# Optimization experiments

Hardware: AMD Instinct MI355X
Metric: run time of the kernel (lower is better)

Reference implementation:

```python
import jax, jax.numpy as jnp
import numpy as np

N, E, NG = 50000, 800000, 256          # nodes, edges, graphs
NODE, EDGE, HID, OUT = 64, 16, 64, 1   # feature dims
NUM_LAYERS = 3


def _lin(key, fan_in, fan_out):
    # torch Linear default init: U(-1/sqrt(fan_in), 1/sqrt(fan_in))
    kw, kb = jax.random.split(key)
    bound = 1.0 / np.sqrt(fan_in)
    W = jax.random.uniform(kw, (fan_in, fan_out), jnp.float32, -bound, bound)
    b = jax.random.uniform(kb, (fan_out,), jnp.float32, -bound, bound)
    return W, b


def setup_inputs() -> dict:
    key = jax.random.key(0)
    ks = jax.random.split(key, 8)
    x = jax.random.normal(ks[0], (N, NODE), jnp.float32)
    edge_attr = jax.random.normal(ks[1], (E, EDGE), jnp.float32)
    edge_index = jax.random.randint(ks[2], (2, E), 0, N, dtype=jnp.int32)
    batch = jnp.sort(jax.random.randint(ks[3], (N,), 0, NG, dtype=jnp.int32))
    W_nh, b_nh = _lin(ks[4], NODE, HID)                 # node_to_hidden
    W_mh, b_mh = _lin(ks[5], 2 * HID + EDGE, HID)       # message_to_hidden
    W_om, b_om = _lin(ks[6], 2 * HID + NODE, HID)       # outMsgLin
    W_out, b_out = _lin(ks[7], HID, OUT)                # outLin
    return {"x": x, "edge_attr": edge_attr,
            "W_nh": W_nh, "b_nh": b_nh, "W_mh": W_mh, "b_mh": b_mh,
            "W_om": W_om, "b_om": b_om, "W_out": W_out, "b_out": b_out,
            "edge_index": edge_index, "batch": batch}


def reference(x, edge_attr, W_nh, b_nh, W_mh, b_mh, W_om, b_om, W_out, b_out,
              edge_index, batch):
    # h0 = relu(node_to_hidden(x))
    h0 = jax.nn.relu(x @ W_nh + b_nh)                      # [N, HID]

    # add_self_loops: append N self edges, self-loop edge_attr filled with 1.0
    self_idx = jnp.arange(N, dtype=edge_index.dtype)
    src = jnp.concatenate([edge_index[0], self_idx])       # x_j index (source)
    dst = jnp.concatenate([edge_index[1], self_idx])       # x_i index (target)
    ea = jnp.concatenate([edge_attr,
                          jnp.ones((N, EDGE), edge_attr.dtype)], axis=0)

    # MPN: num_layers of gather-concat -> scatter-add -> linear + h0 -> relu
    h = h0
    for _ in range(NUM_LAYERS):
        msg = jnp.concatenate([h[dst], h[src], ea], axis=1)        # [E+N, 2H+EDGE]
        agg = jax.ops.segment_sum(msg, dst, num_segments=N)        # [N, 2H+EDGE]
        h = jax.nn.relu(agg @ W_mh + b_mh + h0)                    # [N, HID]

    # outMsg: message = concat[h_i, h_j, x_j], aggr add, update identity
    out_msg = jnp.concatenate([h[dst], h[src], x[src]], axis=1)    # [E+N, 2H+NODE]
    agg2 = jax.ops.segment_sum(out_msg, dst, num_segments=N)       # [N, 2H+NODE]

    out = jax.nn.relu(agg2 @ W_om + b_om)                          # [N, HID]
    pooled = jax.ops.segment_sum(out, batch, num_segments=NG)      # [NG, HID]
    return pooled @ W_out + b_out                                  # [NG, OUT]
```

## Files before the change

### kernel.cpp

```cpp
#include <hip/hip_runtime.h>
#include <hip/hip_fp16.h>

#define N_NODES 50000
#define N_EDGES 800000
#define NGRAPH  256
#define FDIM    64
#define EDIM    16
#define NT      (N_NODES / 16)
#define SH      8
#define M8      (N_NODES * SH)
#define NB8     ((M8 + 255) / 256)
#define CH8     ((NB8 + 255) / 256)
#define NBG     ((N_NODES + 31) / 32)

using half8  = __attribute__((ext_vector_type(8))) _Float16;
using float4v = __attribute__((ext_vector_type(4))) float;

__device__ __forceinline__ unsigned hadd2u(unsigned a, unsigned b) {
    __half2 r = __hadd2(__builtin_bit_cast(__half2, a), __builtin_bit_cast(__half2, b));
    return __builtin_bit_cast(unsigned, r);
}
__device__ __forceinline__ unsigned hmul2u(unsigned a, __half2 m) {
    __half2 r = __hmul2(__builtin_bit_cast(__half2, a), m);
    return __builtin_bit_cast(unsigned, r);
}


__global__ void k_count(const int* __restrict__ dst, int* __restrict__ cnt8) {
    int e = blockIdx.x * blockDim.x + threadIdx.x;
    if (e < N_EDGES) atomicAdd(&cnt8[dst[e] * SH + (e & (SH - 1))], 1);
}

__global__ void k_cvt_x(const float* __restrict__ x, __half* __restrict__ x16) {
    int t = blockIdx.x * blockDim.x + threadIdx.x;
    if (t < N_NODES * FDIM) x16[t] = __float2half(x[t]);
}

__global__ void k_blksum(const int* __restrict__ cnt8, int* __restrict__ blksum) {
    __shared__ int red[4];
    int b = blockIdx.x, t = threadIdx.x;
    int idx = b * 256 + t;
    int s = (idx < M8) ? cnt8[idx] : 0;
#pragma unroll
    for (int off = 32; off > 0; off >>= 1) s += __shfl_down(s, off, 64);
    int lane = t & 63, wid = t >> 6;
    if (lane == 0) red[wid] = s;
    __syncthreads();
    if (t == 0) blksum[b] = red[0] + red[1] + red[2] + red[3];
}

__global__ void k_scanblk(const int* __restrict__ blksum, int* __restrict__ boff,
                          int* __restrict__ rowp8) {
    __shared__ int sh[256];
    int t = threadIdx.x;
    int base = t * CH8;
    int v[CH8];
    int s = 0;
#pragma unroll
    for (int i = 0; i < CH8; i++) {
        int idx = base + i;
        v[i] = (idx < NB8) ? blksum[idx] : 0;
        s += v[i];
    }
    sh[t] = s;
    __syncthreads();
    for (int off = 1; off < 256; off <<= 1) {
        int u = (t >= off) ? sh[t - off] : 0;
        __syncthreads();
        sh[t] += u;
        __syncthreads();
    }
    int run = (t == 0) ? 0 : sh[t - 1];
#pragma unroll
    for (int i = 0; i < CH8; i++) {
        int idx = base + i;
        if (idx < NB8) boff[idx] = run;
        run += v[i];
    }
    if (t == 255) rowp8[M8] = sh[255];
}

__global__ void k_rowp(const int* __restrict__ cnt8, const int* __restrict__ boff,
                       int* __restrict__ rowp8, int* __restrict__ cur8) {
    __shared__ int sh[256];
    int b = blockIdx.x, t = threadIdx.x;
    int idx = b * 256 + t;
    int v = (idx < M8) ? cnt8[idx] : 0;
    sh[t] = v;
    __syncthreads();
    for (int off = 1; off < 256; off <<= 1) {
        int u = (t >= off) ? sh[t - off] : 0;
        __syncthreads();
        sh[t] += u;
        __syncthreads();
    }
    if (idx < M8) {
        int excl = sh[t] - v + boff[b];
        rowp8[idx] = excl;
        cur8[idx]  = excl;
    }
}

__global__ void k_degf(const int* __restrict__ rowp8, float* __restrict__ degf) {
    int i = blockIdx.x * blockDim.x + threadIdx.x;
    if (i < N_NODES) degf[i] = (float)(rowp8[(i + 1) * SH] - rowp8[i * SH] + 1);
}

__global__ void k_fill(const int* __restrict__ src, const int* __restrict__ dst,
                       int* __restrict__ cur8, int2* __restrict__ colperm) {
    int e = blockIdx.x * blockDim.x + threadIdx.x;
    if (e < N_EDGES) {
        int pos = atomicAdd(&cur8[dst[e] * SH + (e & (SH - 1))], 1);
        colperm[pos] = make_int2(src[e], e);
    }
}


__global__ __launch_bounds__(256, 8) void k_gather(
    const __half* __restrict__ h16,
    const int* __restrict__ rowp8, const int2* __restrict__ colperm,
    __half* __restrict__ agg16) {
    int lane = threadIdx.x & 63, wid = threadIdx.x >> 6;
    int g = lane >> 3;
    int c = lane & 7;
    const uint4* h8 = (const uint4*)h16;
    int node = (blockIdx.x * 4 + wid) * 8 + g;
    if (node >= N_NODES) return;
    int beg = rowp8[node * SH], end = rowp8[(node + 1) * SH];
    float a0 = 0, a1 = 0, a2 = 0, a3 = 0, a4 = 0, a5 = 0, a6 = 0, a7 = 0;
    for (int p = beg; p < end; p += 8) {
        int cidx = p + c; if (cidx > end - 1) cidx = end - 1;
        int vj = colperm[cidx].x;
#pragma unroll
        for (int k = 0; k < 8; k++) {
            int j = __shfl(vj, g * 8 + k, 64);
            if (p + k < end) {
                uint4 v = h8[(size_t)j * 8 + c];
                float2 f0 = __half22float2(__builtin_bit_cast(__half2, v.x));
                float2 f1 = __half22float2(__builtin_bit_cast(__half2, v.y));
                float2 f2 = __half22float2(__builtin_bit_cast(__half2, v.z));
                float2 f3 = __half22float2(__builtin_bit_cast(__half2, v.w));
                a0 += f0.x; a1 += f0.y; a2 += f1.x; a3 += f1.y;
                a4 += f2.x; a5 += f2.y; a6 += f3.x; a7 += f3.y;
            }
        }
    }
    uint4 o;
    o.x = __builtin_bit_cast(unsigned, __floats2half2_rn(a0, a1));
    o.y = __builtin_bit_cast(unsigned, __floats2half2_rn(a2, a3));
    o.z = __builtin_bit_cast(unsigned, __floats2half2_rn(a4, a5));
    o.w = __builtin_bit_cast(unsigned, __floats2half2_rn(a6, a7));
    ((uint4*)agg16)[(size_t)node * 8 + c] = o;
}

__global__ __launch_bounds__(256, 8) void k_ea_agg(
    const float* __restrict__ edge_attr,
    const int* __restrict__ rowp8, const int2* __restrict__ colperm,
    float* __restrict__ ea) {
    int lane = threadIdx.x & 63, wid = threadIdx.x >> 6;
    int g = lane >> 3;
    int c = lane & 7;
    const float2* a2p = (const float2*)edge_attr;
    int node = (blockIdx.x * 4 + wid) * 8 + g;
    if (node >= N_NODES) return;
    int beg = rowp8[node * SH], end = rowp8[(node + 1) * SH];
    float x0 = 0.f, x1 = 0.f;
    for (int p = beg; p < end; p += 8) {
        int cidx = p + c; if (cidx > end - 1) cidx = end - 1;
        int vj = colperm[cidx].y;
#pragma unroll
        for (int k = 0; k < 8; k++) {
            int e = __shfl(vj, g * 8 + k, 64);
            if (p + k < end) {
                float2 v = a2p[(size_t)e * 8 + c];
                x0 += v.x; x1 += v.y;
            }
        }
    }
    ((float2*)ea)[(size_t)node * 8 + c] = make_float2(x0, x1);
}

__global__ void k_h0base(const float* __restrict__ x, const float* __restrict__ ea,
                         const float* __restrict__ Wnh, const float* __restrict__ bnh,
                         const float* __restrict__ Wmh, const float* __restrict__ bmh,
                         __half* __restrict__ h0out16, __half* __restrict__ base16) {
    __shared__ __align__(16) float sx[4][FDIM];
    __shared__ __align__(16) float sea[4][EDIM];
    int lane = threadIdx.x & 63;
    int wid  = threadIdx.x >> 6;
    float wnh[FDIM], w3[EDIM];
#pragma unroll
    for (int m = 0; m < FDIM; m++) wnh[m] = Wnh[m * FDIM + lane];
    float csum = 0.f;
#pragma unroll
    for (int m = 0; m < EDIM; m++) {
        w3[m] = Wmh[(2 * FDIM + m) * FDIM + lane];
        csum += w3[m];
    }
    float bnhk = bnh[lane], bmhk = bmh[lane];
    int gw = blockIdx.x * 4 + wid;
    int nw = gridDim.x * 4;
    for (int i = gw; i < N_NODES; i += nw) {
        sx[wid][lane] = x[i * FDIM + lane];
        if (lane < EDIM) sea[wid][lane] = ea[i * EDIM + lane];
        float acc0 = bnhk, acc1 = 0.f, acc2 = 0.f, acc3 = 0.f;
        const float4* s4 = (const float4*)sx[wid];
#pragma unroll
        for (int m4 = 0; m4 < FDIM / 4; m4++) {
            float4 v = s4[m4];
            acc0 = fmaf(v.x, wnh[4 * m4 + 0], acc0);
            acc1 = fmaf(v.y, wnh[4 * m4 + 1], acc1);
            acc2 = fmaf(v.z, wnh[4 * m4 + 2], acc2);
            acc3 = fmaf(v.w, wnh[4 * m4 + 3], acc3);
        }
        float h0 = fmaxf((acc0 + acc2) + (acc1 + acc3), 0.f);
        float b0 = h0 + bmhk + csum, b1 = 0.f, b2 = 0.f, b3 = 0.f;
        const float4* e4 = (const float4*)sea[wid];
#pragma unroll
        for (int m4 = 0; m4 < EDIM / 4; m4++) {
            float4 v = e4[m4];
            b0 = fmaf(v.x, w3[4 * m4 + 0], b0);
            b1 = fmaf(v.y, w3[4 * m4 + 1], b1);
            b2 = fmaf(v.z, w3[4 * m4 + 2], b2);
            b3 = fmaf(v.w, w3[4 * m4 + 3], b3);
        }
        h0out16[i * FDIM + lane] = __float2half(h0);
        base16[i * FDIM + lane]  = __float2half((b0 + b2) + (b1 + b3));
    }
}

#define SROW 136

__global__ __launch_bounds__(256, 4) void k_mv_mfma(
    const __half* __restrict__ agg16, const __half* __restrict__ hin16,
    const __half* __restrict__ base16, const float* __restrict__ degf,
    const float* __restrict__ Wmh, __half* __restrict__ hout16) {
    __shared__ __align__(16) _Float16 S[4][16 * SROW];
    int lane = threadIdx.x & 63, wid = threadIdx.x >> 6;
    int n = lane & 15, quad = lane >> 4;
    half8 bfr[4][4];
#pragma unroll
    for (int kk = 0; kk < 4; kk++)
#pragma unroll
        for (int nn = 0; nn < 4; nn++) {
            half8 tmp;
#pragma unroll
            for (int j = 0; j < 8; j++) {
                int kp = kk * 32 + quad * 8 + j;
                int krow = (kp < 64) ? (64 + kp) : (kp - 64);
                tmp[j] = (_Float16)Wmh[krow * FDIM + nn * 16 + n];
            }
            bfr[kk][nn] = tmp;
        }
    int t = blockIdx.x * 4 + wid;
    if (t >= NT) return;
    int tb = t * 16;
    {
        int m = lane >> 2, c = lane & 3;
        int node = tb + m;
        const uint4* ag4 = (const uint4*)agg16;
        const uint4* hh4 = (const uint4*)hin16;
        uint4 agA = ag4[(size_t)node * 8 + c * 2];
        uint4 agB = ag4[(size_t)node * 8 + c * 2 + 1];
        uint4 hA  = hh4[(size_t)node * 8 + c * 2];
        uint4 hB  = hh4[(size_t)node * 8 + c * 2 + 1];
        __half dh = __float2half(degf[node]);
        __half2 dh2 = __halves2half2(dh, dh);
        uint4 s2A, s2B, s1A, s1B;
        s2A.x = hadd2u(agA.x, hA.x); s2A.y = hadd2u(agA.y, hA.y);
        s2A.z = hadd2u(agA.z, hA.z); s2A.w = hadd2u(agA.w, hA.w);
        s2B.x = hadd2u(agB.x, hB.x); s2B.y = hadd2u(agB.y, hB.y);
        s2B.z = hadd2u(agB.z, hB.z); s2B.w = hadd2u(agB.w, hB.w);
        s1A.x = hmul2u(hA.x, dh2); s1A.y = hmul2u(hA.y, dh2);
        s1A.z = hmul2u(hA.z, dh2); s1A.w = hmul2u(hA.w, dh2);
        s1B.x = hmul2u(hB.x, dh2); s1B.y = hmul2u(hB.y, dh2);
        s1B.z = hmul2u(hB.z, dh2); s1B.w = hmul2u(hB.w, dh2);
        uint4* Sw = (uint4*)(&S[wid][m * SROW]);
        Sw[c * 2]     = s2A;
        Sw[c * 2 + 1] = s2B;
        Sw[8 + c * 2]     = s1A;
        Sw[8 + c * 2 + 1] = s1B;
    }
    float4v acc[4];
#pragma unroll
    for (int nn = 0; nn < 4; nn++)
#pragma unroll
        for (int r = 0; r < 4; r++)
            acc[nn][r] = __half2float(base16[(size_t)(tb + quad * 4 + r) * FDIM + nn * 16 + n]);
    const _Float16* Sr = S[wid];
#pragma unroll
    for (int kk = 0; kk < 4; kk++) {
        half8 a = *(const half8*)(Sr + (lane & 15) * SROW + kk * 32 + quad * 8);
#pragma unroll
        for (int nn = 0; nn < 4; nn++)
            acc[nn] = __builtin_amdgcn_mfma_f32_16x16x32_f16(a, bfr[kk][nn], acc[nn], 0, 0, 0);
    }
#pragma unroll
    for (int nn = 0; nn < 4; nn++)
#pragma unroll
        for (int r = 0; r < 4; r++)
            hout16[(size_t)(tb + quad * 4 + r) * FDIM + nn * 16 + n] =
                __float2half(fmaxf(acc[nn][r], 0.f));
}

__global__ __launch_bounds__(256, 4) void k_out_mv_mfma(
    const __half* __restrict__ agg16, const __half* __restrict__ hin16,
    const __half* __restrict__ obase16, const float* __restrict__ degf,
    const float* __restrict__ Wom, const float* __restrict__ Wout,
    float* __restrict__ sc) {
    __shared__ __align__(16) _Float16 S[4][16 * SROW];
    int lane = threadIdx.x & 63, wid = threadIdx.x >> 6;
    int n = lane & 15, quad = lane >> 4;
    half8 bfr[4][4];
#pragma unroll
    for (int kk = 0; kk < 4; kk++)
#pragma unroll
        for (int nn = 0; nn < 4; nn++) {
            half8 tmp;
#pragma unroll
            for (int j = 0; j < 8; j++) {
                int kp = kk * 32 + quad * 8 + j;
                int krow = (kp < 64) ? (64 + kp) : (kp - 64);
                tmp[j] = (_Float16)Wom[krow * FDIM + nn * 16 + n];
            }
            bfr[kk][nn] = tmp;
        }
    float wo0 = Wout[n], wo1 = Wout[16 + n], wo2 = Wout[32 + n], wo3 = Wout[48 + n];
    int t = blockIdx.x * 4 + wid;
    if (t >= NT) return;
    int tb = t * 16;
    {
        int m = lane >> 2, c = lane & 3;
        int node = tb + m;
        const uint4* ag4 = (const uint4*)agg16;
        const uint4* hh4 = (const uint4*)hin16;
        uint4 agA = ag4[(size_t)node * 8 + c * 2];
        uint4 agB = ag4[(size_t)node * 8 + c * 2 + 1];
        uint4 hA  = hh4[(size_t)node * 8 + c * 2];
        uint4 hB  = hh4[(size_t)node * 8 + c * 2 + 1];
        __half dh = __float2half(degf[node]);
        __half2 dh2 = __halves2half2(dh, dh);
        uint4 s2A, s2B, s1A, s1B;
        s2A.x = hadd2u(agA.x, hA.x); s2A.y = hadd2u(agA.y, hA.y);
        s2A.z = hadd2u(agA.z, hA.z); s2A.w = hadd2u(agA.w, hA.w);
        s2B.x = hadd2u(agB.x, hB.x); s2B.y = hadd2u(agB.y, hB.y);
        s2B.z = hadd2u(agB.z, hB.z); s2B.w = hadd2u(agB.w, hB.w);
        s1A.x = hmul2u(hA.x, dh2); s1A.y = hmul2u(hA.y, dh2);
        s1A.z = hmul2u(hA.z, dh2); s1A.w = hmul2u(hA.w, dh2);
        s1B.x = hmul2u(hB.x, dh2); s1B.y = hmul2u(hB.y, dh2);
        s1B.z = hmul2u(hB.z, dh2); s1B.w = hmul2u(hB.w, dh2);
        uint4* Sw = (uint4*)(&S[wid][m * SROW]);
        Sw[c * 2]     = s2A;
        Sw[c * 2 + 1] = s2B;
        Sw[8 + c * 2]     = s1A;
        Sw[8 + c * 2 + 1] = s1B;
    }
    float4v acc[4];
#pragma unroll
    for (int nn = 0; nn < 4; nn++)
#pragma unroll
        for (int r = 0; r < 4; r++)
            acc[nn][r] = __half2float(obase16[(size_t)(tb + quad * 4 + r) * FDIM + nn * 16 + n]);
    const _Float16* Sr = S[wid];
#pragma unroll
    for (int kk = 0; kk < 4; kk++) {
        half8 a = *(const half8*)(Sr + (lane & 15) * SROW + kk * 32 + quad * 8);
#pragma unroll
        for (int nn = 0; nn < 4; nn++)
            acc[nn] = __builtin_amdgcn_mfma_f32_16x16x32_f16(a, bfr[kk][nn], acc[nn], 0, 0, 0);
    }
#pragma unroll
    for (int r = 0; r < 4; r++) {
        float s = fmaxf(acc[0][r], 0.f) * wo0 + fmaxf(acc[1][r], 0.f) * wo1
                + fmaxf(acc[2][r], 0.f) * wo2 + fmaxf(acc[3][r], 0.f) * wo3;
        s += __shfl_xor(s, 1, 64);
        s += __shfl_xor(s, 2, 64);
        s += __shfl_xor(s, 4, 64);
        s += __shfl_xor(s, 8, 64);
        if (n == 0) sc[tb + quad * 4 + r] = s;
    }
}

#define SROW2 72
__global__ __launch_bounds__(256, 4) void k_obase_mfma(
    const __half* __restrict__ aggX16, const __half* __restrict__ x16,
    const float* __restrict__ Wom, const float* __restrict__ bom,
    __half* __restrict__ obase16) {
    __shared__ __align__(16) _Float16 S[4][16 * SROW2];
    int lane = threadIdx.x & 63, wid = threadIdx.x >> 6;
    int n = lane & 15, quad = lane >> 4;
    half8 bfr[2][4];
#pragma unroll
    for (int kk = 0; kk < 2; kk++)
#pragma unroll
        for (int nn = 0; nn < 4; nn++) {
            half8 tmp;
#pragma unroll
            for (int j = 0; j < 8; j++) {
                int kp = kk * 32 + quad * 8 + j;
                tmp[j] = (_Float16)Wom[(128 + kp) * FDIM + nn * 16 + n];
            }
            bfr[kk][nn] = tmp;
        }
    float bom_n[4];
#pragma unroll
    for (int nn = 0; nn < 4; nn++) bom_n[nn] = bom[nn * 16 + n];
    int t = blockIdx.x * 4 + wid;
    if (t >= NT) return;
    int tb = t * 16;
    {
        int m = lane >> 2, c = lane & 3;
        int node = tb + m;
        const uint4* ag4 = (const uint4*)aggX16;
        const uint4* xx4 = (const uint4*)x16;
        uint4 agA = ag4[(size_t)node * 8 + c * 2];
        uint4 agB = ag4[(size_t)node * 8 + c * 2 + 1];
        uint4 xA  = xx4[(size_t)node * 8 + c * 2];
        uint4 xB  = xx4[(size_t)node * 8 + c * 2 + 1];
        uint4 sA, sB;
        sA.x = hadd2u(agA.x, xA.x); sA.y = hadd2u(agA.y, xA.y);
        sA.z = hadd2u(agA.z, xA.z); sA.w = hadd2u(agA.w, xA.w);
        sB.x = hadd2u(agB.x, xB.x); sB.y = hadd2u(agB.y, xB.y);
        sB.z = hadd2u(agB.z, xB.z); sB.w = hadd2u(agB.w, xB.w);
        uint4* Sw = (uint4*)(&S[wid][m * SROW2]);
        Sw[c * 2]     = sA;
        Sw[c * 2 + 1] = sB;
    }
    float4v acc[4];
#pragma unroll
    for (int nn = 0; nn < 4; nn++)
#pragma unroll
        for (int r = 0; r < 4; r++) acc[nn][r] = bom_n[nn];
    const _Float16* Sr = S[wid];
#pragma unroll
    for (int kk = 0; kk < 2; kk++) {
        half8 a = *(const half8*)(Sr + (lane & 15) * SROW2 + kk * 32 + quad * 8);
#pragma unroll
        for (int nn = 0; nn < 4; nn++)
            acc[nn] = __builtin_amdgcn_mfma_f32_16x16x32_f16(a, bfr[kk][nn], acc[nn], 0, 0, 0);
    }
#pragma unroll
    for (int nn = 0; nn < 4; nn++)
#pragma unroll
        for (int r = 0; r < 4; r++)
            obase16[(size_t)(tb + quad * 4 + r) * FDIM + nn * 16 + n] =
                __float2half(acc[nn][r]);
}

__global__ void k_pool(const float* __restrict__ sc, const int* __restrict__ batch,
                       const float* __restrict__ b_out, float* __restrict__ out) {
    __shared__ float red[4];
    int g = blockIdx.x, t = threadIdx.x;
    int lo = 0, hi = N_NODES;
    while (lo < hi) { int mid = (lo + hi) >> 1; if (batch[mid] < g) lo = mid + 1; else hi = mid; }
    int lo2 = lo, hi2 = N_NODES;
    while (lo2 < hi2) { int mid = (lo2 + hi2) >> 1; if (batch[mid] < g + 1) lo2 = mid + 1; else hi2 = mid; }
    float s = 0.f;
    for (int i = lo + t; i < lo2; i += 256) s += sc[i];
#pragma unroll
    for (int off = 32; off > 0; off >>= 1) s += __shfl_down(s, off, 64);
    int lane = t & 63, wid = t >> 6;
    if (lane == 0) red[wid] = s;
    __syncthreads();
    if (t == 0) out[g] = red[0] + red[1] + red[2] + red[3] + b_out[0];
}


extern "C" void kernel_launch(void* const* d_in, const int* in_sizes, int n_in,
                              void* d_out, int out_size, void* d_ws, size_t ws_size,
                              hipStream_t stream) {
    const float* x         = (const float*)d_in[0];
    const float* edge_attr = (const float*)d_in[1];
    const float* Wnh       = (const float*)d_in[2];
    const float* bnh       = (const float*)d_in[3];
    const float* Wmh       = (const float*)d_in[4];
    const float* bmh       = (const float*)d_in[5];
    const float* Wom       = (const float*)d_in[6];
    const float* bom       = (const float*)d_in[7];
    const float* Wout      = (const float*)d_in[8];
    const float* bout      = (const float*)d_in[9];
    const int*   eidx      = (const int*)d_in[10];
    const int*   batch     = (const int*)d_in[11];
    const int*   srcI = eidx;
    const int*   dstI = eidx + N_EDGES;
    float* out = (float*)d_out;
    (void)in_sizes; (void)n_in; (void)out_size;

    char* w = (char*)d_ws;
    size_t off = 0;
    auto take = [&](size_t b) -> void* {
        void* p = w + off;
        off = (off + b + 255) & ~(size_t)255;
        return p;
    };
    float*  ea     = (float*)take((size_t)N_NODES * EDIM * 4);
    int*    cnt8   = (int*)take((size_t)M8 * 4);
    int*    rowp8  = (int*)take((size_t)(M8 + 1) * 4);
    int*    cur8   = (int*)take((size_t)M8 * 4);
    float*  degf   = (float*)take((size_t)N_NODES * 4);
    int2*   colperm= (int2*)take((size_t)N_EDGES * 8);
    float*  sc     = (float*)take((size_t)N_NODES * 4);
    int*    blks   = (int*)take((size_t)NB8 * 4);
    int*    boff   = (int*)take((size_t)NB8 * 4);
    __half* x16    = (__half*)take((size_t)N_NODES * FDIM * 2);
    __half* hA16   = (__half*)take((size_t)N_NODES * FDIM * 2);
    __half* hB16   = (__half*)take((size_t)N_NODES * FDIM * 2);
    __half* agg16  = (__half*)take((size_t)N_NODES * FDIM * 2);
    __half* base16 = (__half*)take((size_t)N_NODES * FDIM * 2);
    __half* obase16= (__half*)take((size_t)N_NODES * FDIM * 2);
    (void)ws_size;

    const int MVG = (NT + 3) / 4;
    const int GBG = (NBG + 0);

    hipMemsetAsync(cnt8, 0, (size_t)M8 * 4, stream);
    k_count<<<(N_EDGES + 255) / 256, 256, 0, stream>>>(dstI, cnt8);
    k_cvt_x<<<(N_NODES * FDIM + 255) / 256, 256, 0, stream>>>(x, x16);
    k_blksum<<<NB8, 256, 0, stream>>>(cnt8, blks);
    k_scanblk<<<1, 256, 0, stream>>>(blks, boff, rowp8);
    k_rowp<<<NB8, 256, 0, stream>>>(cnt8, boff, rowp8, cur8);
    k_degf<<<(N_NODES + 255) / 256, 256, 0, stream>>>(rowp8, degf);
    k_fill<<<(N_EDGES + 255) / 256, 256, 0, stream>>>(srcI, dstI, cur8, colperm);

    k_gather<<<GBG, 256, 0, stream>>>(x16, rowp8, colperm, agg16);
    k_obase_mfma<<<MVG, 256, 0, stream>>>(agg16, x16, Wom, bom, obase16);
    k_ea_agg<<<GBG, 256, 0, stream>>>(edge_attr, rowp8, colperm, ea);
    k_h0base<<<2048, 256, 0, stream>>>(x, ea, Wnh, bnh, Wmh, bmh, hA16, base16);

    k_gather<<<GBG, 256, 0, stream>>>(hA16, rowp8, colperm, agg16);
    k_mv_mfma<<<MVG, 256, 0, stream>>>(agg16, hA16, base16, degf, Wmh, hB16);

    k_gather<<<GBG, 256, 0, stream>>>(hB16, rowp8, colperm, agg16);
    k_mv_mfma<<<MVG, 256, 0, stream>>>(agg16, hB16, base16, degf, Wmh, hA16);

    k_gather<<<GBG, 256, 0, stream>>>(hA16, rowp8, colperm, agg16);
    k_mv_mfma<<<MVG, 256, 0, stream>>>(agg16, hA16, base16, degf, Wmh, hB16);

    k_gather<<<GBG, 256, 0, stream>>>(hB16, rowp8, colperm, agg16);
    k_out_mv_mfma<<<MVG, 256, 0, stream>>>(agg16, hB16, obase16, degf, Wom, Wout, sc);
    k_pool<<<NGRAPH, 256, 0, stream>>>(sc, batch, bout, out);
}
```

Before: 393.0 us.

## Partition count and fill atomics by destination range across block groups

k_count and k_fill now launch eight groups of blocks. Each group scans all edges but only performs atomics for destinations inside its own node range, and the block index interleaves the group (blockIdx & 7). The intent is to localize atomic traffic, perhaps so each group's counters stay in one XCD's L2 cache. The cost is that the dst array is read eight times over, and the filter adds branch divergence.

```diff
diff --git a/kernel.cpp b/kernel.cpp
--- a/kernel.cpp
+++ b/kernel.cpp
@@ -13,6 +13,11 @@
 #define CH8     ((NB8 + 255) / 256)
 #define NBG     ((N_NODES + 31) / 32)
 
+#define GRPS       8
+#define GRP_BLOCKS 256
+#define GRID_CF    (GRPS * GRP_BLOCKS)
+#define NPG        ((N_NODES + GRPS - 1) / GRPS)
+
 using half8  = __attribute__((ext_vector_type(8))) _Float16;
 using float4v = __attribute__((ext_vector_type(4))) float;
 
@@ -26,9 +31,16 @@
 }
 
 
-__global__ void k_count(const int* __restrict__ dst, int* __restrict__ cnt8) {
-    int e = blockIdx.x * blockDim.x + threadIdx.x;
-    if (e < N_EDGES) atomicAdd(&cnt8[dst[e] * SH + (e & (SH - 1))], 1);
+__global__ __launch_bounds__(256) void k_count(const int* __restrict__ dst,
+                                               int* __restrict__ cnt8) {
+    int grp = blockIdx.x & (GRPS - 1);
+    int bi  = blockIdx.x >> 3;
+    int lo = grp * NPG;
+    int hi = lo + NPG; if (hi > N_NODES) hi = N_NODES;
+    for (int e = bi * 256 + threadIdx.x; e < N_EDGES; e += GRP_BLOCKS * 256) {
+        int d = dst[e];
+        if (d >= lo && d < hi) atomicAdd(&cnt8[d * SH + (e & (SH - 1))], 1);
+    }
 }
 
 __global__ void k_cvt_x(const float* __restrict__ x, __half* __restrict__ x16) {
@@ -106,12 +118,20 @@
     if (i < N_NODES) degf[i] = (float)(rowp8[(i + 1) * SH] - rowp8[i * SH] + 1);
 }
 
-__global__ void k_fill(const int* __restrict__ src, const int* __restrict__ dst,
-                       int* __restrict__ cur8, int2* __restrict__ colperm) {
-    int e = blockIdx.x * blockDim.x + threadIdx.x;
-    if (e < N_EDGES) {
-        int pos = atomicAdd(&cur8[dst[e] * SH + (e & (SH - 1))], 1);
-        colperm[pos] = make_int2(src[e], e);
+__global__ __launch_bounds__(256) void k_fill(const int* __restrict__ src,
+                                              const int* __restrict__ dst,
+                                              int* __restrict__ cur8,
+                                              int2* __restrict__ colperm) {
+    int grp = blockIdx.x & (GRPS - 1);
+    int bi  = blockIdx.x >> 3;
+    int lo = grp * NPG;
+    int hi = lo + NPG; if (hi > N_NODES) hi = N_NODES;
+    for (int e = bi * 256 + threadIdx.x; e < N_EDGES; e += GRP_BLOCKS * 256) {
+        int d = dst[e];
+        if (d >= lo && d < hi) {
+            int pos = atomicAdd(&cur8[d * SH + (e & (SH - 1))], 1);
+            colperm[pos] = make_int2(src[e], e);
+        }
     }
 }
 
@@ -514,13 +534,13 @@
     const int GBG = (NBG + 0);
 
     hipMemsetAsync(cnt8, 0, (size_t)M8 * 4, stream);
-    k_count<<<(N_EDGES + 255) / 256, 256, 0, stream>>>(dstI, cnt8);
+    k_count<<<GRID_CF, 256, 0, stream>>>(dstI, cnt8);
     k_cvt_x<<<(N_NODES * FDIM + 255) / 256, 256, 0, stream>>>(x, x16);
     k_blksum<<<NB8, 256, 0, stream>>>(cnt8, blks);
     k_scanblk<<<1, 256, 0, stream>>>(blks, boff, rowp8);
     k_rowp<<<NB8, 256, 0, stream>>>(cnt8, boff, rowp8, cur8);
     k_degf<<<(N_NODES + 255) / 256, 256, 0, stream>>>(rowp8, degf);
-    k_fill<<<(N_EDGES + 255) / 256, 256, 0, stream>>>(srcI, dstI, cur8, colperm);
+    k_fill<<<GRID_CF, 256, 0, stream>>>(srcI, dstI, cur8, colperm);
 
     k_gather<<<GBG, 256, 0, stream>>>(x16, rowp8, colperm, agg16);
     k_obase_mfma<<<MVG, 256, 0, stream>>>(agg16, x16, Wom, bom, obase16);
```

New measurement: 379.9 us. -3.3%, faster.
